# Kernel tuning notes

Hardware: AMD Instinct MI355X
Metric: run time of the kernel (lower is better)

Reference implementation:

```python
import jax, jax.numpy as jnp
import numpy as np

NUM_HEADS = 12
EPS = 1e-12  # F.normalize default eps


def setup_inputs() -> dict:
    key = jax.random.key(0)
    ks = jax.random.split(key, 6)
    B, N, C, M = 32, 1024, 768, 64
    s = 1.0 / np.sqrt(C)
    return {
        "x": jax.random.normal(ks[0], (B, N, C), jnp.float32),
        "Wc": jax.random.normal(ks[1], (M, C), jnp.float32) * s,
        "bc": jnp.zeros((M,), jnp.float32),
        "Wq": jax.random.normal(ks[2], (C, C), jnp.float32) * s,
        "bq": jnp.zeros((C,), jnp.float32),
        "Wk": jax.random.normal(ks[3], (C, C), jnp.float32) * s,
        "bk": jnp.zeros((C,), jnp.float32),
        "Wv": jax.random.normal(ks[4], (C, C), jnp.float32) * s,
        "bv": jnp.zeros((C,), jnp.float32),
        "Wp": jax.random.normal(ks[5], (C, C), jnp.float32) * s,
        "bp": jnp.zeros((C,), jnp.float32),
    }


def reference(x, Wc, bc, Wq, bq, Wk, bk, Wv, bv, Wp, bp):
    B, N, C = x.shape
    H = NUM_HEADS
    D = C // H
    scale = D ** -0.5

    # Cluster: linear -> transpose -> sigmoid/N -> einsum -> L2 norm
    c = jnp.einsum('bnc,mc->bmn', x, Wc) + bc[None, :, None]   # (B, M, N)
    c = jax.nn.sigmoid(c) / N
    z = jnp.einsum('bmn,bnc->bmc', c, x)                        # (B, M, C)
    z = z / jnp.maximum(jnp.linalg.norm(z, axis=-1, keepdims=True), EPS)

    M = z.shape[1]
    q = (x @ Wq.T + bq).reshape(B, N, H, D).transpose(0, 2, 1, 3)  # (B,H,N,D)
    k = (z @ Wk.T + bk).reshape(B, M, H, D).transpose(0, 2, 1, 3)  # (B,H,M,D)
    v = (z @ Wv.T + bv).reshape(B, M, H, D).transpose(0, 2, 1, 3)  # (B,H,M,D)

    attn = jax.nn.softmax(jnp.einsum('bhnd,bhmd->bhnm', q, k) * scale, axis=-1)
    o = jnp.einsum('bhnm,bhmd->bhnd', attn, v)                  # (B,H,N,D)
    o = o.transpose(0, 2, 1, 3).reshape(B, N, C)
    return o @ Wp.T + bp
```

## Files before the change

### kernel.cpp

```cpp
#include <hip/hip_runtime.h>
#include <hip/hip_bf16.h>
#include <cstdint>

#define BB 32
#define NN 1024
#define CC 768
#define MM 64
#define HH 12
#define DD 64

typedef float f4v __attribute__((ext_vector_type(4)));
typedef __bf16 bf8 __attribute__((ext_vector_type(8)));
typedef __bf16 bf4 __attribute__((ext_vector_type(4)));

__device__ __forceinline__ f4v mfma16(bf8 a, bf8 b, f4v c) {
    return __builtin_amdgcn_mfma_f32_16x16x32_bf16(a, b, c, 0, 0, 0);
}
__device__ __forceinline__ __bf16 f2bf(float f) { return (__bf16)f; }

__device__ __forceinline__ void gl2lds16(const void* g, void* lds) {
    __builtin_amdgcn_global_load_lds((const __attribute__((address_space(1))) void*)g,
                                     (__attribute__((address_space(3))) void*)lds, 16, 0, 0);
}

__global__ __launch_bounds__(256) void k_cvtW(
        const float* __restrict__ Wc, const float* __restrict__ Wq,
        const float* __restrict__ Wk, const float* __restrict__ Wv,
        const float* __restrict__ Wp,
        __bf16* __restrict__ wc, __bf16* __restrict__ wq,
        __bf16* __restrict__ wk, __bf16* __restrict__ wv,
        __bf16* __restrict__ wp) {
    const float* in; __bf16* out; int n4;
    switch (blockIdx.y) {
        case 0: in = Wc; out = wc; n4 = MM * CC / 4; break;
        case 1: in = Wq; out = wq; n4 = CC * CC / 4; break;
        case 2: in = Wk; out = wk; n4 = CC * CC / 4; break;
        case 3: in = Wv; out = wv; n4 = CC * CC / 4; break;
        default: in = Wp; out = wp; n4 = CC * CC / 4; break;
    }
    int i = blockIdx.x * 256 + threadIdx.x;
    if (i < n4) {
        float4 v = *(const float4*)&in[i * 4];
        bf4 o; o[0] = f2bf(v.x); o[1] = f2bf(v.y); o[2] = f2bf(v.z); o[3] = f2bf(v.w);
        *(bf4*)&out[i * 4] = o;
    }
}

#define TS 80
__global__ __launch_bounds__(256) void k_cvtx(const float* __restrict__ x,
        __bf16* __restrict__ xb, __bf16* __restrict__ xt) {
    int c0 = blockIdx.x * 64, n0 = blockIdx.y * 64, b = blockIdx.z;
    __shared__ __align__(16) __bf16 tile[64 * TS];
    int t = threadIdx.x;
#pragma unroll
    for (int i = 0; i < 4; i++) {
        int idx = t + 256 * i, r = idx >> 4, cq = idx & 15;
        float4 v = *(const float4*)&x[((size_t)(b * NN + n0 + r)) * CC + c0 + cq * 4];
        __bf16* d = &tile[r * TS + cq * 4];
        d[0] = f2bf(v.x); d[1] = f2bf(v.y); d[2] = f2bf(v.z); d[3] = f2bf(v.w);
    }
    __syncthreads();
#pragma unroll
    for (int i = 0; i < 2; i++) {
        int idx = t + 256 * i, r = idx >> 3, ch = idx & 7;
        *(bf8*)&xb[((size_t)(b * NN + n0 + r)) * CC + c0 + ch * 8] = *(const bf8*)&tile[r * TS + ch * 8];
    }
#pragma unroll
    for (int i = 0; i < 2; i++) {
        int idx = t + 256 * i, c = idx >> 3, ch = idx & 7;
        bf8 v;
#pragma unroll
        for (int j = 0; j < 8; j++) v[j] = tile[(ch * 8 + j) * TS + c];
        *(bf8*)&xt[((size_t)(b * CC + c0 + c)) * NN + n0 + ch * 8] = v;
    }
}

__global__ __launch_bounds__(256) void k_cluster(const __bf16* __restrict__ xb,
        const __bf16* __restrict__ Wc, const float* __restrict__ bc,
        __bf16* __restrict__ cbmn) {
    int n0 = blockIdx.x * 128, b = blockIdx.y;
    int t = threadIdx.x, w = t >> 6, l = t & 63, quad = l >> 4, l16 = l & 15;
    f4v acc[2][4];
#pragma unroll
    for (int i = 0; i < 2; i++) for (int j = 0; j < 4; j++) acc[i][j] = (f4v)0.0f;
    for (int k0 = 0; k0 < CC; k0 += 32) {
        bf8 afr[2], bfr[4];
#pragma unroll
        for (int sr = 0; sr < 2; sr++)
            afr[sr] = *(const bf8*)&xb[((size_t)(b * NN + n0 + w * 32 + sr * 16 + l16)) * CC + k0 + quad * 8];
#pragma unroll
        for (int sc = 0; sc < 4; sc++)
            bfr[sc] = *(const bf8*)&Wc[(size_t)(sc * 16 + l16) * CC + k0 + quad * 8];
#pragma unroll
        for (int sr = 0; sr < 2; sr++)
#pragma unroll
            for (int sc = 0; sc < 4; sc++)
                acc[sr][sc] = mfma16(afr[sr], bfr[sc], acc[sr][sc]);
    }
#pragma unroll
    for (int sr = 0; sr < 2; sr++)
#pragma unroll
        for (int sc = 0; sc < 4; sc++) {
            int m = sc * 16 + l16;
            float bias = bc[m];
            bf4 p;
#pragma unroll
            for (int r = 0; r < 4; r++) {
                float val = acc[sr][sc][r] + bias;
                val = 1.0f / (1.0f + __expf(-val));
                p[r] = f2bf(val * (1.0f / 1024.0f));
            }
            *(bf4*)&cbmn[((size_t)(b * MM + m)) * NN + n0 + w * 32 + sr * 16 + quad * 4] = p;
        }
}

__global__ __launch_bounds__(256) void k_z(const __bf16* __restrict__ cbmn,
        const __bf16* __restrict__ xt, float* __restrict__ z) {
    int c0 = blockIdx.x * 64, b = blockIdx.y;
    int t = threadIdx.x, w = t >> 6, l = t & 63, quad = l >> 4, l16 = l & 15;
    f4v acc[4];
#pragma unroll
    for (int j = 0; j < 4; j++) acc[j] = (f4v)0.0f;
    for (int n0 = 0; n0 < NN; n0 += 32) {
        bf8 afr = *(const bf8*)&cbmn[((size_t)(b * MM + w * 16 + l16)) * NN + n0 + quad * 8];
#pragma unroll
        for (int sc = 0; sc < 4; sc++) {
            bf8 bfr = *(const bf8*)&xt[((size_t)(b * CC + c0 + sc * 16 + l16)) * NN + n0 + quad * 8];
            acc[sc] = mfma16(afr, bfr, acc[sc]);
        }
    }
#pragma unroll
    for (int sc = 0; sc < 4; sc++) {
        int cc = c0 + sc * 16 + l16;
#pragma unroll
        for (int r = 0; r < 4; r++) {
            int m = w * 16 + quad * 4 + r;
            z[((size_t)(b * MM + m)) * CC + cc] = acc[sc][r];
        }
    }
}

__global__ __launch_bounds__(256) void k_znorm(const float* __restrict__ z, __bf16* __restrict__ zb) {
    int w = threadIdx.x >> 6, l = threadIdx.x & 63;
    int row = blockIdx.x * 4 + w;
    const float* zr = &z[(size_t)row * CC];
    float v[12]; float ss = 0.f;
#pragma unroll
    for (int i = 0; i < 12; i++) { v[i] = zr[l + i * 64]; ss += v[i] * v[i]; }
#pragma unroll
    for (int off = 32; off; off >>= 1) ss += __shfl_xor(ss, off);
    float s = 1.0f / fmaxf(sqrtf(ss), 1e-12f);
    __bf16* zo = &zb[(size_t)row * CC];
#pragma unroll
    for (int i = 0; i < 12; i++) zo[l + i * 64] = f2bf(v[i] * s);
}

__global__ __launch_bounds__(256) void k_kv(const __bf16* __restrict__ zb,
        const __bf16* __restrict__ Wk, const float* __restrict__ bk,
        const __bf16* __restrict__ Wv, const float* __restrict__ bv,
        __bf16* __restrict__ kout, __bf16* __restrict__ vtout) {
    int ct = blockIdx.x, b = blockIdx.y, which = blockIdx.z;
    const __bf16* W = which ? Wv : Wk;
    const float* bias = which ? bv : bk;
    int t = threadIdx.x, w = t >> 6, l = t & 63, quad = l >> 4, l16 = l & 15;
    f4v acc[4][2];
#pragma unroll
    for (int i = 0; i < 4; i++) for (int j = 0; j < 2; j++) acc[i][j] = (f4v)0.0f;
    for (int k0 = 0; k0 < CC; k0 += 32) {
        bf8 afr[4], bfr[2];
#pragma unroll
        for (int sr = 0; sr < 4; sr++)
            afr[sr] = *(const bf8*)&zb[((size_t)(b * MM + sr * 16 + l16)) * CC + k0 + quad * 8];
#pragma unroll
        for (int sc = 0; sc < 2; sc++)
            bfr[sc] = *(const bf8*)&W[((size_t)(ct * 128 + w * 32 + sc * 16 + l16)) * CC + k0 + quad * 8];
#pragma unroll
        for (int sr = 0; sr < 4; sr++)
#pragma unroll
            for (int sc = 0; sc < 2; sc++)
                acc[sr][sc] = mfma16(afr[sr], bfr[sc], acc[sr][sc]);
    }
#pragma unroll
    for (int sr = 0; sr < 4; sr++)
#pragma unroll
        for (int sc = 0; sc < 2; sc++) {
            int col = ct * 128 + w * 32 + sc * 16 + l16;
            float bb = bias[col];
            int h = col >> 6, d = col & 63;
            if (which == 0) {
#pragma unroll
                for (int r = 0; r < 4; r++) {
                    int m = sr * 16 + quad * 4 + r;
                    kout[(((size_t)(b * HH + h)) * MM + m) * DD + d] = f2bf(acc[sr][sc][r] + bb);
                }
            } else {
                bf4 p;
#pragma unroll
                for (int r = 0; r < 4; r++) p[r] = f2bf(acc[sr][sc][r] + bb);
                *(bf4*)&vtout[(((size_t)(b * HH + h)) * DD + d) * MM + sr * 16 + quad * 4] = p;
            }
        }
}

#define STAGE_AB(Asrc, Bsrc, dstbase, kk)                                                             \
    do {                                                                                              \
        __bf16* _Ad = (dstbase);                                                                      \
        int _row = w * 16 + (l >> 2), _ch = l & 3;                                                    \
        gl2lds16(&(Asrc)[(arow0 + _row) * CC + (kk) + _ch * 8], &_Ad[w * 512]);                       \
        gl2lds16(&(Asrc)[(arow0 + 64 + _row) * CC + (kk) + _ch * 8], &_Ad[2048 + w * 512]);           \
        gl2lds16(&(Bsrc)[((size_t)(jt * 128) + _row) * CC + (kk) + _ch * 8], &_Ad[4096 + w * 512]);   \
        gl2lds16(&(Bsrc)[((size_t)(jt * 128) + 64 + _row) * CC + (kk) + _ch * 8], &_Ad[4096 + 2048 + w * 512]); \
    } while (0)

__global__ __launch_bounds__(256, 4) void k_qproj(const __bf16* __restrict__ xb,
        const __bf16* __restrict__ Wq, const float* __restrict__ bq,
        __bf16* __restrict__ qb) {
    int orig = blockIdx.y * gridDim.x + blockIdx.x;
    int lid = (orig & 7) * 192 + (orig >> 3);
    int jt = lid % 6;
    size_t arow0 = (size_t)(lid / 6) * 128;

    __shared__ __align__(16) __bf16 smem[4 * 128 * 32];
    int t = threadIdx.x, w = t >> 6, l = t & 63, quad = l >> 4, l16 = l & 15;
    int wr = w & 1, wc = w >> 1;
    f4v acc[4][4];
#pragma unroll
    for (int i = 0; i < 4; i++) for (int j = 0; j < 4; j++) acc[i][j] = (f4v)0.0f;

    STAGE_AB(xb, Wq, smem, 0);
    asm volatile("s_waitcnt vmcnt(0)" ::: "memory");
    __builtin_amdgcn_s_barrier();

    for (int kt = 0; kt < 24; ++kt) {
        int cur = kt & 1;
        if (kt < 23) STAGE_AB(xb, Wq, smem + (cur ^ 1) * 8192, (kt + 1) * 32);
        const __bf16* As = smem + cur * 8192;
        const __bf16* Bs = As + 4096;
        bf8 afr[4], bfr[4];
#pragma unroll
        for (int sr = 0; sr < 4; sr++) afr[sr] = *(const bf8*)&As[(wr * 64 + sr * 16 + l16) * 32 + quad * 8];
#pragma unroll
        for (int sc = 0; sc < 4; sc++) bfr[sc] = *(const bf8*)&Bs[(wc * 64 + sc * 16 + l16) * 32 + quad * 8];
        __builtin_amdgcn_s_setprio(1);
#pragma unroll
        for (int sr = 0; sr < 4; sr++)
#pragma unroll
            for (int sc = 0; sc < 4; sc++)
                acc[sr][sc] = mfma16(afr[sr], bfr[sc], acc[sr][sc]);
        __builtin_amdgcn_s_setprio(0);
        if (kt < 23) asm volatile("s_waitcnt vmcnt(0)" ::: "memory");
        __builtin_amdgcn_s_barrier();
    }

    __bf16* eb = smem;
    for (int p = 0; p < 2; ++p) {
        if (wc == p) {
#pragma unroll
            for (int sc = 0; sc < 4; sc++) {
                int col = jt * 128 + p * 64 + sc * 16 + l16;
                float bb = bq[col];
#pragma unroll
                for (int sr = 0; sr < 4; sr++)
#pragma unroll
                    for (int r = 0; r < 4; r++)
                        eb[(wr * 64 + sr * 16 + quad * 4 + r) * 72 + sc * 16 + l16] = f2bf(acc[sr][sc][r] + bb);
            }
        }
        __syncthreads();
#pragma unroll
        for (int i = 0; i < 4; i++) {
            int idx = t + 256 * i, row = idx >> 3, ch = idx & 7;
            *(bf8*)&qb[(arow0 + row) * CC + jt * 128 + p * 64 + ch * 8] = *(const bf8*)&eb[row * 72 + ch * 8];
        }
        __syncthreads();
    }
}

#define QS 72
__global__ __launch_bounds__(256) void k_attn(const __bf16* __restrict__ qb,
        const __bf16* __restrict__ kb, const __bf16* __restrict__ vt,
        __bf16* __restrict__ ob) {
    int n0 = blockIdx.x * 128, h = blockIdx.y, b = blockIdx.z;
    __shared__ __align__(16) __bf16 ps[128 * QS];
    int t = threadIdx.x, w = t >> 6, l = t & 63, quad = l >> 4, l16 = l & 15;
    size_t bh = (size_t)(b * HH + h);

    f4v sacc[2][4];
#pragma unroll
    for (int i = 0; i < 2; i++) for (int j = 0; j < 4; j++) sacc[i][j] = (f4v)0.0f;
#pragma unroll
    for (int kc = 0; kc < 2; kc++) {
        bf8 afr[2], bfr[4];
#pragma unroll
        for (int sr = 0; sr < 2; sr++)
            afr[sr] = *(const bf8*)&qb[((size_t)(b * NN + n0 + w * 32 + sr * 16 + l16)) * CC + h * 64 + kc * 32 + quad * 8];
#pragma unroll
        for (int sc = 0; sc < 4; sc++)
            bfr[sc] = *(const bf8*)&kb[(bh * MM + sc * 16 + l16) * DD + kc * 32 + quad * 8];
#pragma unroll
        for (int sr = 0; sr < 2; sr++)
#pragma unroll
            for (int sc = 0; sc < 4; sc++)
                sacc[sr][sc] = mfma16(afr[sr], bfr[sc], sacc[sr][sc]);
    }
#pragma unroll
    for (int sr = 0; sr < 2; sr++) {
#pragma unroll
        for (int r = 0; r < 4; r++) {
            float mx = -1e30f;
#pragma unroll
            for (int sc = 0; sc < 4; sc++) mx = fmaxf(mx, sacc[sr][sc][r] * 0.125f);
#pragma unroll
            for (int off = 1; off < 16; off <<= 1) mx = fmaxf(mx, __shfl_xor(mx, off));
            float e[4]; float sum = 0.f;
#pragma unroll
            for (int sc = 0; sc < 4; sc++) { e[sc] = __expf(sacc[sr][sc][r] * 0.125f - mx); sum += e[sc]; }
#pragma unroll
            for (int off = 1; off < 16; off <<= 1) sum += __shfl_xor(sum, off);
            float inv = 1.0f / sum;
            int row = w * 32 + sr * 16 + quad * 4 + r;
#pragma unroll
            for (int sc = 0; sc < 4; sc++) ps[row * QS + sc * 16 + l16] = f2bf(e[sc] * inv);
        }
    }
    f4v oacc[2][4];
#pragma unroll
    for (int i = 0; i < 2; i++) for (int j = 0; j < 4; j++) oacc[i][j] = (f4v)0.0f;
#pragma unroll
    for (int kc = 0; kc < 2; kc++) {
        bf8 afr[2], bfr[4];
#pragma unroll
        for (int sr = 0; sr < 2; sr++)
            afr[sr] = *(const bf8*)&ps[(w * 32 + sr * 16 + l16) * QS + kc * 32 + quad * 8];
#pragma unroll
        for (int sc = 0; sc < 4; sc++)
            bfr[sc] = *(const bf8*)&vt[(bh * DD + sc * 16 + l16) * MM + kc * 32 + quad * 8];
#pragma unroll
        for (int sr = 0; sr < 2; sr++)
#pragma unroll
            for (int sc = 0; sc < 4; sc++)
                oacc[sr][sc] = mfma16(afr[sr], bfr[sc], oacc[sr][sc]);
    }
#pragma unroll
    for (int sr = 0; sr < 2; sr++)
#pragma unroll
        for (int sc = 0; sc < 4; sc++) {
            int row = w * 32 + sr * 16;
#pragma unroll
            for (int r = 0; r < 4; r++)
                ps[(row + quad * 4 + r) * QS + sc * 16 + l16] = f2bf(oacc[sr][sc][r]);
        }
    __syncthreads();
#pragma unroll
    for (int i = 0; i < 4; i++) {
        int idx = t + 256 * i, row = idx >> 3, ch = idx & 7;
        *(bf8*)&ob[((size_t)(b * NN + n0 + row)) * CC + h * 64 + ch * 8] = *(const bf8*)&ps[row * QS + ch * 8];
    }
}

__global__ __launch_bounds__(256, 4) void k_oproj(const __bf16* __restrict__ ob,
        const __bf16* __restrict__ Wp, const float* __restrict__ bp,
        float* __restrict__ out) {
    int orig = blockIdx.y * gridDim.x + blockIdx.x;
    int lid = (orig & 7) * 192 + (orig >> 3);
    int jt = lid % 6;
    size_t arow0 = (size_t)(lid / 6) * 128;

    __shared__ __align__(16) char smem_raw[128 * 68 * 4];
    __bf16* smem = (__bf16*)smem_raw;
    int t = threadIdx.x, w = t >> 6, l = t & 63, quad = l >> 4, l16 = l & 15;
    int wr = w & 1, wc = w >> 1;
    f4v acc[4][4];
#pragma unroll
    for (int i = 0; i < 4; i++) for (int j = 0; j < 4; j++) acc[i][j] = (f4v)0.0f;

    STAGE_AB(ob, Wp, smem, 0);
    asm volatile("s_waitcnt vmcnt(0)" ::: "memory");
    __builtin_amdgcn_s_barrier();

    for (int kt = 0; kt < 24; ++kt) {
        int cur = kt & 1;
        if (kt < 23) STAGE_AB(ob, Wp, smem + (cur ^ 1) * 8192, (kt + 1) * 32);
        const __bf16* As = smem + cur * 8192;
        const __bf16* Bs = As + 4096;
        bf8 afr[4], bfr[4];
#pragma unroll
        for (int sr = 0; sr < 4; sr++) afr[sr] = *(const bf8*)&As[(wr * 64 + sr * 16 + l16) * 32 + quad * 8];
#pragma unroll
        for (int sc = 0; sc < 4; sc++) bfr[sc] = *(const bf8*)&Bs[(wc * 64 + sc * 16 + l16) * 32 + quad * 8];
        __builtin_amdgcn_s_setprio(1);
#pragma unroll
        for (int sr = 0; sr < 4; sr++)
#pragma unroll
            for (int sc = 0; sc < 4; sc++)
                acc[sr][sc] = mfma16(afr[sr], bfr[sc], acc[sr][sc]);
        __builtin_amdgcn_s_setprio(0);
        if (kt < 23) asm volatile("s_waitcnt vmcnt(0)" ::: "memory");
        __builtin_amdgcn_s_barrier();
    }

    float* eb = (float*)smem_raw;
    for (int p = 0; p < 2; ++p) {
        if (wc == p) {
#pragma unroll
            for (int sc = 0; sc < 4; sc++) {
                int col = jt * 128 + p * 64 + sc * 16 + l16;
                float bb = bp[col];
#pragma unroll
                for (int sr = 0; sr < 4; sr++)
#pragma unroll
                    for (int r = 0; r < 4; r++)
                        eb[(wr * 64 + sr * 16 + quad * 4 + r) * 68 + sc * 16 + l16] = acc[sr][sc][r] + bb;
            }
        }
        __syncthreads();
#pragma unroll
        for (int i = 0; i < 8; i++) {
            int idx = t + 256 * i, row = idx >> 4, c4 = idx & 15;
            *(float4*)&out[(arow0 + row) * CC + jt * 128 + p * 64 + c4 * 4] = *(const float4*)&eb[row * 68 + c4 * 4];
        }
        __syncthreads();
    }
}

extern "C" void kernel_launch(void* const* d_in, const int* in_sizes, int n_in,
                              void* d_out, int out_size, void* d_ws, size_t ws_size,
                              hipStream_t stream) {
    (void)in_sizes; (void)n_in; (void)out_size; (void)ws_size;
    const float* x  = (const float*)d_in[0];
    const float* Wc = (const float*)d_in[1];
    const float* bc = (const float*)d_in[2];
    const float* Wq = (const float*)d_in[3];
    const float* bq = (const float*)d_in[4];
    const float* Wk = (const float*)d_in[5];
    const float* bk = (const float*)d_in[6];
    const float* Wv = (const float*)d_in[7];
    const float* bv = (const float*)d_in[8];
    const float* Wp = (const float*)d_in[9];
    const float* bp = (const float*)d_in[10];
    float* out = (float*)d_out;

    char* ws = (char*)d_ws;
    size_t off = 0;
    auto alloc = [&](size_t bytes) { void* p = ws + off; off = (off + bytes + 255) & ~(size_t)255; return p; };
    __bf16* wc_b = (__bf16*)alloc((size_t)MM * CC * 2);
    __bf16* wq_b = (__bf16*)alloc((size_t)CC * CC * 2);
    __bf16* wk_b = (__bf16*)alloc((size_t)CC * CC * 2);
    __bf16* wv_b = (__bf16*)alloc((size_t)CC * CC * 2);
    __bf16* wp_b = (__bf16*)alloc((size_t)CC * CC * 2);
    __bf16* xb   = (__bf16*)alloc((size_t)BB * NN * CC * 2);
    __bf16* xt_o = (__bf16*)alloc((size_t)BB * NN * CC * 2);
    __bf16* q_b  = (__bf16*)alloc((size_t)BB * NN * CC * 2);
    __bf16* c_bmn= (__bf16*)alloc((size_t)BB * MM * NN * 2);
    float*  z_f  = (float*) alloc((size_t)BB * MM * CC * 4);
    __bf16* z_b  = (__bf16*)alloc((size_t)BB * MM * CC * 2);
    __bf16* k_b  = (__bf16*)alloc((size_t)BB * HH * MM * DD * 2);
    __bf16* v_t  = (__bf16*)alloc((size_t)BB * HH * MM * DD * 2);

    k_cvtW<<<dim3((CC * CC / 4 + 255) / 256, 5), 256, 0, stream>>>(
        Wc, Wq, Wk, Wv, Wp, wc_b, wq_b, wk_b, wv_b, wp_b);

    k_cvtx<<<dim3(CC / 64, NN / 64, BB), 256, 0, stream>>>(x, xb, xt_o);
    k_cluster<<<dim3(NN / 128, BB), 256, 0, stream>>>(xb, wc_b, bc, c_bmn);
    k_z<<<dim3(CC / 64, BB), 256, 0, stream>>>(c_bmn, xt_o, z_f);
    k_znorm<<<(BB * MM) / 4, 256, 0, stream>>>(z_f, z_b);
    k_kv<<<dim3(CC / 128, BB, 2), 256, 0, stream>>>(z_b, wk_b, bk, wv_b, bv, k_b, v_t);
    k_qproj<<<dim3(CC / 128, (BB * NN) / 128), 256, 0, stream>>>(xb, wq_b, bq, q_b);
    k_attn<<<dim3(NN / 128, HH, BB), 256, 0, stream>>>(q_b, k_b, v_t, xt_o );
    k_oproj<<<dim3(CC / 128, (BB * NN) / 128), 256, 0, stream>>>(xt_o, wp_b, bp, out);
}
```

Before: 281.1 us.

## Triple-buffer GEMM K-loop with partial waitcnt and XOR-swizzled LDS layout

The Q and output projection GEMMs now use a three-stage LDS ring, prefetching two K tiles ahead and waiting with vmcnt(8) instead of draining all loads every iteration. The global-to-LDS chunk index and the fragment read index are XOR-swizzled to cut LDS bank conflicts on the bf8 reads. LDS per block grows to three stages, so launch bounds drop from 4 to 3 blocks per CU, which lowers occupancy. The loop is fully unrolled through a shared macro.

Result: faster. 271.4 us (-3.5%).

```diff
diff --git a/kernel.cpp b/kernel.cpp
--- a/kernel.cpp
+++ b/kernel.cpp
@@ -205,14 +205,43 @@
 #define STAGE_AB(Asrc, Bsrc, dstbase, kk)                                                             \
     do {                                                                                              \
         __bf16* _Ad = (dstbase);                                                                      \
-        int _row = w * 16 + (l >> 2), _ch = l & 3;                                                    \
+        int _row = w * 16 + (l >> 2), _ch = (l & 3) ^ ((l >> 3) & 3);                                 \
         gl2lds16(&(Asrc)[(arow0 + _row) * CC + (kk) + _ch * 8], &_Ad[w * 512]);                       \
         gl2lds16(&(Asrc)[(arow0 + 64 + _row) * CC + (kk) + _ch * 8], &_Ad[2048 + w * 512]);           \
         gl2lds16(&(Bsrc)[((size_t)(jt * 128) + _row) * CC + (kk) + _ch * 8], &_Ad[4096 + w * 512]);   \
         gl2lds16(&(Bsrc)[((size_t)(jt * 128) + 64 + _row) * CC + (kk) + _ch * 8], &_Ad[4096 + 2048 + w * 512]); \
     } while (0)
 
-__global__ __launch_bounds__(256, 4) void k_qproj(const __bf16* __restrict__ xb,
+#define GEMM_KLOOP(Asrc, Bsrc)                                                                        \
+    STAGE_AB(Asrc, Bsrc, smem, 0);                                                                    \
+    STAGE_AB(Asrc, Bsrc, smem + 8192, 32);                                                            \
+    _Pragma("unroll")                                                                                 \
+    for (int kt = 0; kt < 24; ++kt) {                                                                 \
+        if (kt < 22) STAGE_AB(Asrc, Bsrc, smem + ((kt + 2) % 3) * 8192, (kt + 2) * 32);               \
+        if (kt < 22)      asm volatile("s_waitcnt vmcnt(8)" ::: "memory");                            \
+        else if (kt == 22) asm volatile("s_waitcnt vmcnt(4)" ::: "memory");                           \
+        else               asm volatile("s_waitcnt vmcnt(0)" ::: "memory");                           \
+        __builtin_amdgcn_s_barrier();                                                                 \
+        const __bf16* As = smem + (kt % 3) * 8192;                                                    \
+        const __bf16* Bs = As + 4096;                                                                 \
+        bf8 afr[4], bfr[4];                                                                           \
+        _Pragma("unroll")                                                                             \
+        for (int sr = 0; sr < 4; sr++)                                                                \
+            afr[sr] = *(const bf8*)&As[(wr * 64 + sr * 16 + l16) * 32 + swz * 8];                     \
+        _Pragma("unroll")                                                                             \
+        for (int sc = 0; sc < 4; sc++)                                                                \
+            bfr[sc] = *(const bf8*)&Bs[(wc * 64 + sc * 16 + l16) * 32 + swz * 8];                     \
+        __builtin_amdgcn_s_setprio(1);                                                                \
+        _Pragma("unroll")                                                                             \
+        for (int sr = 0; sr < 4; sr++)                                                                \
+            _Pragma("unroll")                                                                         \
+            for (int sc = 0; sc < 4; sc++)                                                            \
+                acc[sr][sc] = mfma16(afr[sr], bfr[sc], acc[sr][sc]);                                  \
+        __builtin_amdgcn_s_setprio(0);                                                                \
+        __builtin_amdgcn_s_barrier();                                                                 \
+    }
+
+__global__ __launch_bounds__(256, 3) void k_qproj(const __bf16* __restrict__ xb,
         const __bf16* __restrict__ Wq, const float* __restrict__ bq,
         __bf16* __restrict__ qb) {
     int orig = blockIdx.y * gridDim.x + blockIdx.x;
@@ -220,37 +249,15 @@
     int jt = lid % 6;
     size_t arow0 = (size_t)(lid / 6) * 128;
 
-    __shared__ __align__(16) __bf16 smem[4 * 128 * 32];
+    __shared__ __align__(16) __bf16 smem[3 * 8192];
     int t = threadIdx.x, w = t >> 6, l = t & 63, quad = l >> 4, l16 = l & 15;
     int wr = w & 1, wc = w >> 1;
+    int swz = quad ^ ((l16 >> 1) & 3);
     f4v acc[4][4];
 #pragma unroll
     for (int i = 0; i < 4; i++) for (int j = 0; j < 4; j++) acc[i][j] = (f4v)0.0f;
 
-    STAGE_AB(xb, Wq, smem, 0);
-    asm volatile("s_waitcnt vmcnt(0)" ::: "memory");
-    __builtin_amdgcn_s_barrier();
-
-    for (int kt = 0; kt < 24; ++kt) {
-        int cur = kt & 1;
-        if (kt < 23) STAGE_AB(xb, Wq, smem + (cur ^ 1) * 8192, (kt + 1) * 32);
-        const __bf16* As = smem + cur * 8192;
-        const __bf16* Bs = As + 4096;
-        bf8 afr[4], bfr[4];
-#pragma unroll
-        for (int sr = 0; sr < 4; sr++) afr[sr] = *(const bf8*)&As[(wr * 64 + sr * 16 + l16) * 32 + quad * 8];
-#pragma unroll
-        for (int sc = 0; sc < 4; sc++) bfr[sc] = *(const bf8*)&Bs[(wc * 64 + sc * 16 + l16) * 32 + quad * 8];
-        __builtin_amdgcn_s_setprio(1);
-#pragma unroll
-        for (int sr = 0; sr < 4; sr++)
-#pragma unroll
-            for (int sc = 0; sc < 4; sc++)
-                acc[sr][sc] = mfma16(afr[sr], bfr[sc], acc[sr][sc]);
-        __builtin_amdgcn_s_setprio(0);
-        if (kt < 23) asm volatile("s_waitcnt vmcnt(0)" ::: "memory");
-        __builtin_amdgcn_s_barrier();
-    }
+    GEMM_KLOOP(xb, Wq);
 
     __bf16* eb = smem;
     for (int p = 0; p < 2; ++p) {
@@ -358,7 +365,7 @@
     }
 }
 
-__global__ __launch_bounds__(256, 4) void k_oproj(const __bf16* __restrict__ ob,
+__global__ __launch_bounds__(256, 3) void k_oproj(const __bf16* __restrict__ ob,
         const __bf16* __restrict__ Wp, const float* __restrict__ bp,
         float* __restrict__ out) {
     int orig = blockIdx.y * gridDim.x + blockIdx.x;
@@ -366,40 +373,17 @@
     int jt = lid % 6;
     size_t arow0 = (size_t)(lid / 6) * 128;
 
-    __shared__ __align__(16) char smem_raw[128 * 68 * 4];
-    __bf16* smem = (__bf16*)smem_raw;
+    __shared__ __align__(16) __bf16 smem[3 * 8192];
     int t = threadIdx.x, w = t >> 6, l = t & 63, quad = l >> 4, l16 = l & 15;
     int wr = w & 1, wc = w >> 1;
+    int swz = quad ^ ((l16 >> 1) & 3);
     f4v acc[4][4];
 #pragma unroll
     for (int i = 0; i < 4; i++) for (int j = 0; j < 4; j++) acc[i][j] = (f4v)0.0f;
 
-    STAGE_AB(ob, Wp, smem, 0);
-    asm volatile("s_waitcnt vmcnt(0)" ::: "memory");
-    __builtin_amdgcn_s_barrier();
-
-    for (int kt = 0; kt < 24; ++kt) {
-        int cur = kt & 1;
-        if (kt < 23) STAGE_AB(ob, Wp, smem + (cur ^ 1) * 8192, (kt + 1) * 32);
-        const __bf16* As = smem + cur * 8192;
-        const __bf16* Bs = As + 4096;
-        bf8 afr[4], bfr[4];
-#pragma unroll
-        for (int sr = 0; sr < 4; sr++) afr[sr] = *(const bf8*)&As[(wr * 64 + sr * 16 + l16) * 32 + quad * 8];
-#pragma unroll
-        for (int sc = 0; sc < 4; sc++) bfr[sc] = *(const bf8*)&Bs[(wc * 64 + sc * 16 + l16) * 32 + quad * 8];
-        __builtin_amdgcn_s_setprio(1);
-#pragma unroll
-        for (int sr = 0; sr < 4; sr++)
-#pragma unroll
-            for (int sc = 0; sc < 4; sc++)
-                acc[sr][sc] = mfma16(afr[sr], bfr[sc], acc[sr][sc]);
-        __builtin_amdgcn_s_setprio(0);
-        if (kt < 23) asm volatile("s_waitcnt vmcnt(0)" ::: "memory");
-        __builtin_amdgcn_s_barrier();
-    }
-
-    float* eb = (float*)smem_raw;
+    GEMM_KLOOP(ob, Wp);
+
+    float* eb = (float*)smem;
     for (int p = 0; p < 2; ++p) {
         if (wc == p) {
 #pragma unroll
```
